# Kernel optimization log

Hardware: AMD Instinct MI355X
Metric: run time of the kernel (lower is better)

Reference implementation:

```python
import jax, jax.numpy as jnp
import numpy as np

B, T, D = 2, 2048, 1024
H, HD = 16, 64
DL, DC = 512, 256
THETA = 10000.0
LN_EPS = 1e-5


def setup_inputs() -> dict:
    key = jax.random.key(0)
    ks = jax.random.split(key, 8)
    s = 0.02
    return {
        "x": jax.random.normal(ks[0], (B, T, D), jnp.float32),
        "W_q": jax.random.normal(ks[1], (H * HD, D), jnp.float32) * s,
        "b_q": jnp.zeros((H * HD,), jnp.float32),
        "W_kvl": jax.random.normal(ks[2], (DL, D), jnp.float32) * s,
        "b_kvl": jnp.zeros((DL,), jnp.float32),
        "ts_scale": jnp.ones((DL,), jnp.float32),
        "ts_shift": jnp.zeros((DL,), jnp.float32),
        "W_comp": jax.random.normal(ks[3], (DC, DL), jnp.float32) * s,
        "W_exp": jax.random.normal(ks[4], (DL, DC), jnp.float32) * s,
        "ln_g": jnp.ones((DC,), jnp.float32),
        "ln_b": jnp.zeros((DC,), jnp.float32),
        "W_fkv": jax.random.normal(ks[5], (2 * H * HD, DL), jnp.float32) * s,
        "b_fkv": jnp.zeros((2 * H * HD,), jnp.float32),
        "W_out": jax.random.normal(ks[6], (D, H * HD), jnp.float32) * s,
        "b_out": jnp.zeros((D,), jnp.float32),
    }


def _rope_tables(t_len):
    inv_freq = 1.0 / (THETA ** (jnp.arange(0, HD, 2, dtype=jnp.float32) / HD))
    pos = jnp.arange(t_len, dtype=jnp.float32)
    freqs = pos[:, None] * inv_freq[None, :]          # [T, HD/2]
    cos = jnp.concatenate([jnp.cos(freqs)] * 2, -1)   # [T, HD]
    sin = jnp.concatenate([jnp.sin(freqs)] * 2, -1)
    return cos[None, None], sin[None, None]           # [1,1,T,HD]


def _rotate_half(z):
    return jnp.concatenate([-z[..., HD // 2:], z[..., :HD // 2]], -1)


def reference(x, W_q, b_q, W_kvl, b_kvl, ts_scale, ts_shift, W_comp, W_exp,
              ln_g, ln_b, W_fkv, b_fkv, W_out, b_out):
    # Q path: [B,T,D] -> [B,H,T,HD]
    q = (jnp.einsum('btd,ed->bte', x, W_q) + b_q).reshape(B, T, H, HD).transpose(0, 2, 1, 3)

    # KV latent + learned KVSplice bottleneck
    kvl = jnp.einsum('btd,ld->btl', x, W_kvl) + b_kvl                 # [B,T,DL]
    xt = kvl * jax.nn.softplus(ts_scale) + ts_shift
    c = jnp.einsum('btl,cl->btc', xt, W_comp)                         # [B,T,DC]
    mu = jnp.mean(c, -1, keepdims=True)
    var = jnp.mean(jnp.square(c - mu), -1, keepdims=True)
    c = (c - mu) * jax.lax.rsqrt(var + LN_EPS) * ln_g + ln_b
    dec = jnp.einsum('btc,lc->btl', c, W_exp)                         # [B,T,DL]

    # Decompress latent to K,V
    kv = jnp.einsum('btl,el->bte', dec, W_fkv) + b_fkv                # [B,T,2*H*HD]
    kv = kv.reshape(B, T, 2, H, HD).transpose(2, 0, 3, 1, 4)          # [2,B,H,T,HD]
    k, v = kv[0], kv[1]

    # RoPE
    cos, sin = _rope_tables(T)
    q = q * cos + _rotate_half(q) * sin
    k = k * cos + _rotate_half(k) * sin

    # Causal SDPA
    scale = 1.0 / np.sqrt(HD)
    scores = jnp.einsum('bhqd,bhkd->bhqk', q, k) * scale
    mask = jnp.tril(jnp.ones((T, T), bool))
    scores = jnp.where(mask, scores, jnp.float32(-1e30))
    attn = jax.nn.softmax(scores, axis=-1)
    o = jnp.einsum('bhqk,bhkd->bhqd', attn, v)
    o = o.transpose(0, 2, 1, 3).reshape(B, T, H * HD)
    return jnp.einsum('bte,de->btd', o, W_out) + b_out
```

## Files before the change

### kernel.cpp

```cpp
#include <hip/hip_runtime.h>
#include <math.h>

#define B_SZ   2
#define T_SEQ  2048
#define NH     16
#define HDIM   64
#define D_MOD  1024
#define DL     512
#define DC     256
#define MROWS  4096

typedef __attribute__((ext_vector_type(8))) short bf16x8;
typedef __attribute__((ext_vector_type(4))) float f32x4;

#define SCALE_Q 0.18033688011112042f
#define PSTR 68

static __device__ __forceinline__ unsigned short f2bf(float f) {
    union { float f; unsigned u; } v; v.f = f;
    unsigned r = v.u + 0x7fffu + ((v.u >> 16) & 1u);
    return (unsigned short)(r >> 16);
}

static __device__ __forceinline__ void gl_lds16(const unsigned short* g,
                                                unsigned short* l) {
    __builtin_amdgcn_global_load_lds(
        (const __attribute__((address_space(1))) unsigned int*)g,
        (__attribute__((address_space(3))) unsigned int*)l, 16, 0, 0);
}

__global__ __launch_bounds__(256) void cvt_bf16(
    const float* __restrict__ x,  const float* __restrict__ wq,
    const float* __restrict__ wkvl, const float* __restrict__ wcomp,
    const float* __restrict__ wexp, const float* __restrict__ wfkv,
    const float* __restrict__ wout,
    unsigned short* __restrict__ xb,  unsigned short* __restrict__ wqh,
    unsigned short* __restrict__ wkvlh, unsigned short* __restrict__ wcomph,
    unsigned short* __restrict__ wexph, unsigned short* __restrict__ wfkvh,
    unsigned short* __restrict__ wouth, float2* __restrict__ rope_tab)
{
    const int g = blockIdx.x * 256 + threadIdx.x;
    const int stride = gridDim.x * 256;
#define CVT_SEG(src, dst, n4)                                              \
    for (int i = g; i < (n4); i += stride) {                               \
        float4 v = ((const float4*)(src))[i];                              \
        unsigned short h[4] = {f2bf(v.x), f2bf(v.y), f2bf(v.z), f2bf(v.w)};\
        *(uint2*)((dst) + (size_t)i * 4) = *(uint2*)h;                     \
    }
    CVT_SEG(x, xb, 1048576)
    CVT_SEG(wq, wqh, 262144)
    CVT_SEG(wkvl, wkvlh, 131072)
    CVT_SEG(wcomp, wcomph, 32768)
    CVT_SEG(wexp, wexph, 32768)
    CVT_SEG(wfkv, wfkvh, 262144)
    CVT_SEG(wout, wouth, 262144)
#undef CVT_SEG
    for (int i = g; i < T_SEQ * 32; i += stride) {
        const int t = i >> 5, fi = i & 31;
        const float inv = __expf((float)fi * (-9.210340371976184f / 32.0f));
        float sn, cs; sincosf((float)t * inv, &sn, &cs);
        rope_tab[i] = make_float2(cs, sn);
    }
}

#define GEMM64R_PROLOG(Aptr, Wptr, Kdim)                                       \
    __shared__ unsigned short As[64 * 32];                                     \
    __shared__ unsigned short Ws[64 * 32];                                     \
    const int tid = threadIdx.x;                                               \
    const int w = tid >> 6, lane = tid & 63;                                   \
    const int l16 = lane & 15, quad = lane >> 4;                               \
    const int srow = lane >> 2, scol = (lane & 3) << 3;                        \
    const unsigned short* Ag = (Aptr) + (size_t)(m0 + w * 16 + srow) * (Kdim) + scol; \
    const unsigned short* Wg = (Wptr) + (size_t)(n0 + w * 16 + srow) * (Kdim) + scol; \
    unsigned short* Al = &As[w * 512];                                         \
    unsigned short* Wl = &Ws[w * 512];                                         \
    f32x4 acc[4];                                                              \
    _Pragma("unroll") for (int j = 0; j < 4; ++j)                              \
        acc[j] = (f32x4){0.f, 0.f, 0.f, 0.f};                                  \
    for (int k0 = 0; k0 < (Kdim); k0 += 32) {                                  \
        __syncthreads();                                                       \
        gl_lds16(Ag + k0, Al);                                                 \
        gl_lds16(Wg + k0, Wl);                                                 \
        __syncthreads();                                                       \
        const bf16x8 af = *(const bf16x8*)&As[(w * 16 + l16) * 32 + quad * 8]; \
        bf16x8 bfr[4];                                                         \
        _Pragma("unroll") for (int j = 0; j < 4; ++j)                          \
            bfr[j] = *(const bf16x8*)&Ws[(j * 16 + l16) * 32 + quad * 8];      \
        _Pragma("unroll") for (int j = 0; j < 4; ++j)                          \
            acc[j] = __builtin_amdgcn_mfma_f32_16x16x32_bf16(af, bfr[j], acc[j], 0, 0, 0); \
    }

__global__ __launch_bounds__(256) void gemm_qxt(
    const unsigned short* __restrict__ A, const unsigned short* __restrict__ Wq,
    const unsigned short* __restrict__ Wkvl,
    const float* __restrict__ b_q, const float* __restrict__ b_kvl,
    const float* __restrict__ ts_scale, const float* __restrict__ ts_shift,
    const float2* __restrict__ tab,
    unsigned short* __restrict__ qh, unsigned short* __restrict__ xt)
{
    const int m0 = blockIdx.x * 64;
    const bool is_q = (blockIdx.y < 16);
    const int n0 = is_q ? blockIdx.y * 64 : (blockIdx.y - 16) * 64;
    const unsigned short* W = is_q ? Wq : Wkvl;

    GEMM64R_PROLOG(A, W, D_MOD)

    if (is_q) {
#pragma unroll
        for (int j = 0; j < 4; ++j) {
            const int col = n0 + j * 16 + l16;
            const int h = col >> 6, hd = col & 63;
            const float bv = b_q[col];
            const float bvp = b_q[col ^ 32];
            const float sgn = (hd < 32) ? -1.f : 1.f;
#pragma unroll
            for (int reg = 0; reg < 4; ++reg) {
                const int row = m0 + w * 16 + quad * 4 + reg;
                const int b = row >> 11, t = row & (T_SEQ - 1);
                const float2 cssn = tab[t * 32 + (hd & 31)];
                const float v  = acc[j][reg] + bv;
                const float vp = acc[j ^ 2][reg] + bvp;
                const float r = (v * cssn.x + sgn * vp * cssn.y) * SCALE_Q;
                qh[(((size_t)b * NH + h) * T_SEQ + t) * HDIM + hd] = f2bf(r);
            }
        }
    } else {
#pragma unroll
        for (int j = 0; j < 4; ++j) {
            const int col = n0 + j * 16 + l16;
            const float bv = b_kvl[col];
            const float sp_s = log1pf(expf(ts_scale[col]));
            const float sp_t = ts_shift[col];
#pragma unroll
            for (int reg = 0; reg < 4; ++reg) {
                const int row = m0 + w * 16 + quad * 4 + reg;
                const float val = (acc[j][reg] + bv) * sp_s + sp_t;
                xt[(size_t)row * DL + col] = f2bf(val);
            }
        }
    }
}

__global__ __launch_bounds__(256) void gemm_kv(
    const unsigned short* __restrict__ A, const unsigned short* __restrict__ W,
    const float* __restrict__ bias, const float2* __restrict__ tab,
    unsigned short* __restrict__ kh, unsigned short* __restrict__ vth)
{
    const int m0 = blockIdx.x * 64, n0 = blockIdx.y * 64;

    GEMM64R_PROLOG(A, W, DL)

    if (n0 < 1024) {
#pragma unroll
        for (int j = 0; j < 4; ++j) {
            const int col = n0 + j * 16 + l16;
            const int h = (col >> 6) & 15, hd = col & 63;
            const float bv = bias[col];
            const float bvp = bias[col ^ 32];
            const float sgn = (hd < 32) ? -1.f : 1.f;
#pragma unroll
            for (int reg = 0; reg < 4; ++reg) {
                const int row = m0 + w * 16 + quad * 4 + reg;
                const int b = row >> 11, t = row & (T_SEQ - 1);
                const float2 cssn = tab[t * 32 + (hd & 31)];
                const float v  = acc[j][reg] + bv;
                const float vp = acc[j ^ 2][reg] + bvp;
                const float r = v * cssn.x + sgn * vp * cssn.y;
                kh[(((size_t)b * NH + h) * T_SEQ + t) * HDIM + hd] = f2bf(r);
            }
        }
    } else {
#pragma unroll
        for (int j = 0; j < 4; ++j) {
            const int col = n0 + j * 16 + l16;
            const int cv = col - 1024;
            const int h = cv >> 6, hd = cv & 63;
            const float bv = bias[col];
            unsigned short hv[4];
            const int r0 = m0 + w * 16 + quad * 4;
            const int b = r0 >> 11, t0 = r0 & (T_SEQ - 1);
#pragma unroll
            for (int reg = 0; reg < 4; ++reg)
                hv[reg] = f2bf(acc[j][reg] + bv);
            *(uint2*)&vth[(((size_t)b * NH + h) * HDIM + hd) * T_SEQ + t0] =
                *(uint2*)hv;
        }
    }
}

__global__ __launch_bounds__(256) void gemm_out(
    const unsigned short* __restrict__ A, const unsigned short* __restrict__ W,
    const float* __restrict__ bias, float* __restrict__ C)
{
    const int m0 = blockIdx.x * 64, n0 = blockIdx.y * 64;

    GEMM64R_PROLOG(A, W, D_MOD)

#pragma unroll
    for (int j = 0; j < 4; ++j) {
        const int col = n0 + j * 16 + l16;
        const float bv = bias[col];
#pragma unroll
        for (int reg = 0; reg < 4; ++reg) {
            const int row = m0 + w * 16 + quad * 4 + reg;
            C[(size_t)row * D_MOD + col] = acc[j][reg] + bv;
        }
    }
}

__global__ __launch_bounds__(256) void gemm_cb(
    const unsigned short* __restrict__ A, const unsigned short* __restrict__ Wc,
    const unsigned short* __restrict__ We,
    const float* __restrict__ g, const float* __restrict__ bta,
    unsigned short* __restrict__ dec)
{
    __shared__ unsigned short As[16 * 32];
    __shared__ unsigned short Ws[256 * 32];
    __shared__ unsigned short Cs[16 * 260];
    __shared__ float redS[4][16];
    __shared__ float redQ[4][16];

    const int tid = threadIdx.x;
    const int w = tid >> 6, lane = tid & 63;
    const int l16 = lane & 15, quad = lane >> 4;
    const int m0 = blockIdx.x * 16;

    const int srow = lane >> 2, scol = (lane & 3) << 3;
    const unsigned short* Ag = A + (size_t)(m0 + srow) * DL + scol;
    const unsigned short* Wg = Wc + (size_t)(w * 64 + srow) * DL + scol;

    f32x4 acc[4];
#pragma unroll
    for (int j = 0; j < 4; ++j) acc[j] = (f32x4){0.f, 0.f, 0.f, 0.f};

    for (int k0 = 0; k0 < DL; k0 += 32) {
        __syncthreads();
        if (w == 0) gl_lds16(Ag + k0, &As[0]);
#pragma unroll
        for (int c = 0; c < 4; ++c)
            gl_lds16(Wg + (size_t)(c * 16) * DL + k0, &Ws[(w * 64 + c * 16) * 32]);
        __syncthreads();

        const bf16x8 af = *(const bf16x8*)&As[l16 * 32 + quad * 8];
        bf16x8 bfr[4];
#pragma unroll
        for (int j = 0; j < 4; ++j)
            bfr[j] = *(const bf16x8*)&Ws[(w * 64 + j * 16 + l16) * 32 + quad * 8];
#pragma unroll
        for (int j = 0; j < 4; ++j)
            acc[j] = __builtin_amdgcn_mfma_f32_16x16x32_bf16(af, bfr[j], acc[j], 0, 0, 0);
    }

    float s[4], q2[4];
#pragma unroll
    for (int reg = 0; reg < 4; ++reg) {
        float sv = (acc[0][reg] + acc[1][reg]) + (acc[2][reg] + acc[3][reg]);
        float qv = (acc[0][reg] * acc[0][reg] + acc[1][reg] * acc[1][reg]) +
                   (acc[2][reg] * acc[2][reg] + acc[3][reg] * acc[3][reg]);
#pragma unroll
        for (int off = 1; off < 16; off <<= 1) {
            sv += __shfl_xor(sv, off);
            qv += __shfl_xor(qv, off);
        }
        s[reg] = sv; q2[reg] = qv;
    }
    if (l16 == 0) {
#pragma unroll
        for (int reg = 0; reg < 4; ++reg) {
            redS[w][quad * 4 + reg] = s[reg];
            redQ[w][quad * 4 + reg] = q2[reg];
        }
    }
    __syncthreads();

#pragma unroll
    for (int reg = 0; reg < 4; ++reg) {
        const int r = quad * 4 + reg;
        const float sum = (redS[0][r] + redS[1][r]) + (redS[2][r] + redS[3][r]);
        const float sq  = (redQ[0][r] + redQ[1][r]) + (redQ[2][r] + redQ[3][r]);
        const float mu  = sum * (1.0f / DC);
        const float var = sq * (1.0f / DC) - mu * mu;
        const float rstd = rsqrtf(var + 1e-5f);
#pragma unroll
        for (int j = 0; j < 4; ++j) {
            const int col = w * 64 + j * 16 + l16;
            const float val = (acc[j][reg] - mu) * rstd * g[col] + bta[col];
            Cs[r * 260 + col] = f2bf(val);
        }
    }
    __syncthreads();

    bf16x8 a2[8];
#pragma unroll
    for (int kk = 0; kk < 8; ++kk)
        a2[kk] = *(const bf16x8*)&Cs[l16 * 260 + kk * 32 + quad * 8];

#pragma unroll
    for (int j = 0; j < 8; ++j) {
        f32x4 acc2 = (f32x4){0.f, 0.f, 0.f, 0.f};
        const unsigned short* Bg = We + (size_t)(w * 128 + j * 16 + l16) * DC + quad * 8;
#pragma unroll
        for (int kk = 0; kk < 8; ++kk) {
            const bf16x8 b2 = *(const bf16x8*)(Bg + kk * 32);
            acc2 = __builtin_amdgcn_mfma_f32_16x16x32_bf16(a2[kk], b2, acc2, 0, 0, 0);
        }
        const int col = w * 128 + j * 16 + l16;
#pragma unroll
        for (int reg = 0; reg < 4; ++reg)
            dec[(size_t)(m0 + quad * 4 + reg) * DL + col] = f2bf(acc2[reg]);
    }
}

__global__ __launch_bounds__(256, 3) void flash_mfma(
    const unsigned short* __restrict__ q, const unsigned short* __restrict__ k,
    const unsigned short* __restrict__ vt, unsigned short* __restrict__ o)
{
    __shared__ unsigned short Ks[64 * 72];
    __shared__ unsigned short Vs[64 * 72];
    __shared__ unsigned short Ps[64 * PSTR];

    const int bh = blockIdx.x & 31;
    const int j  = 31 - (blockIdx.x >> 5);
    const int q0 = j * 64;
    const int tid = threadIdx.x;
    const int w = tid >> 6, lane = tid & 63;
    const int l16 = lane & 15, quad = lane >> 4;
    const int rbase = q0 + w * 16;

    bf16x8 qf[2];
#pragma unroll
    for (int kk = 0; kk < 2; ++kk)
        qf[kk] = *(const bf16x8*)(q + ((size_t)bh * T_SEQ + rbase + l16) * HDIM + kk * 32 + quad * 8);

    f32x4 of[4];
    float lrow[4];
#pragma unroll
    for (int dt = 0; dt < 4; ++dt) of[dt] = (f32x4){0.f, 0.f, 0.f, 0.f};
#pragma unroll
    for (int r = 0; r < 4; ++r) lrow[r] = 0.f;

    const int ldr = tid >> 2;
    const int ldc = (tid & 3) * 16;
    const unsigned short* kgb = k + ((size_t)bh * T_SEQ + ldr) * HDIM + ldc;
    const unsigned short* vgb = vt + ((size_t)bh * HDIM + ldr) * T_SEQ + ldc;

    const int kend = (j + 1) * 64;
    for (int k0 = 0; k0 < kend; k0 += 64) {
        __syncthreads();
        {
            const unsigned short* kg = kgb + (size_t)k0 * HDIM;
            *(bf16x8*)&Ks[ldr * 72 + ldc]     = *(const bf16x8*)kg;
            *(bf16x8*)&Ks[ldr * 72 + ldc + 8] = *(const bf16x8*)(kg + 8);
            const unsigned short* vg = vgb + k0;
            *(bf16x8*)&Vs[ldr * 72 + ldc]     = *(const bf16x8*)vg;
            *(bf16x8*)&Vs[ldr * 72 + ldc + 8] = *(const bf16x8*)(vg + 8);
        }
        __syncthreads();

        bf16x8 kf[4][2];
#pragma unroll
        for (int nt = 0; nt < 4; ++nt)
#pragma unroll
            for (int kk = 0; kk < 2; ++kk)
                kf[nt][kk] = *(const bf16x8*)&Ks[(nt * 16 + l16) * 72 + kk * 32 + quad * 8];

        f32x4 sf[4];
#pragma unroll
        for (int nt = 0; nt < 4; ++nt) {
            sf[nt] = (f32x4){0.f, 0.f, 0.f, 0.f};
#pragma unroll
            for (int kk = 0; kk < 2; ++kk)
                sf[nt] = __builtin_amdgcn_mfma_f32_16x16x32_bf16(qf[kk], kf[nt][kk], sf[nt], 0, 0, 0);
        }

        const bool need_mask = (k0 + 63) > rbase;
#pragma unroll
        for (int reg = 0; reg < 4; ++reg) {
            float a0 = sf[0][reg], a1 = sf[1][reg], a2 = sf[2][reg], a3 = sf[3][reg];
            if (need_mask) {
                const int tq = rbase + quad * 4 + reg;
                if (k0 +      l16 > tq) a0 = -1e30f;
                if (k0 + 16 + l16 > tq) a1 = -1e30f;
                if (k0 + 32 + l16 > tq) a2 = -1e30f;
                if (k0 + 48 + l16 > tq) a3 = -1e30f;
            }
            union { float f; unsigned u; } u0, u1, u2, u3;
            u0.f = exp2f(a0); u1.f = exp2f(a1);
            u2.f = exp2f(a2); u3.f = exp2f(a3);
            const int prow = (w * 16 + quad * 4 + reg) * PSTR + l16;
            Ps[prow]      = (unsigned short)(u0.u >> 16);
            Ps[prow + 16] = (unsigned short)(u1.u >> 16);
            Ps[prow + 32] = (unsigned short)(u2.u >> 16);
            Ps[prow + 48] = (unsigned short)(u3.u >> 16);
            u0.u &= 0xffff0000u; u1.u &= 0xffff0000u;
            u2.u &= 0xffff0000u; u3.u &= 0xffff0000u;
            lrow[reg] += (u0.f + u1.f) + (u2.f + u3.f);
        }

        bf16x8 vf[4][2];
#pragma unroll
        for (int dt = 0; dt < 4; ++dt)
#pragma unroll
            for (int kk = 0; kk < 2; ++kk)
                vf[dt][kk] = *(const bf16x8*)&Vs[(dt * 16 + l16) * 72 + kk * 32 + quad * 8];

        bf16x8 pf[2];
#pragma unroll
        for (int kk = 0; kk < 2; ++kk)
            pf[kk] = *(const bf16x8*)&Ps[(w * 16 + l16) * PSTR + kk * 32 + quad * 8];
#pragma unroll
        for (int dt = 0; dt < 4; ++dt)
#pragma unroll
            for (int kk = 0; kk < 2; ++kk)
                of[dt] = __builtin_amdgcn_mfma_f32_16x16x32_bf16(pf[kk], vf[dt][kk], of[dt], 0, 0, 0);
    }

    const int b = bh >> 4, h = bh & 15;
#pragma unroll
    for (int reg = 0; reg < 4; ++reg) {
        float l = lrow[reg];
        l += __shfl_xor(l, 1);
        l += __shfl_xor(l, 2);
        l += __shfl_xor(l, 4);
        l += __shfl_xor(l, 8);
        const float inv = 1.0f / l;
        const int t = rbase + quad * 4 + reg;
#pragma unroll
        for (int dt = 0; dt < 4; ++dt)
            o[((size_t)b * T_SEQ + t) * (NH * HDIM) + h * HDIM + dt * 16 + l16] =
                f2bf(of[dt][reg] * inv);
    }
}

extern "C" void kernel_launch(void* const* d_in, const int* in_sizes, int n_in,
                              void* d_out, int out_size, void* d_ws, size_t ws_size,
                              hipStream_t stream)
{
    (void)in_sizes; (void)n_in; (void)out_size; (void)ws_size;

    const float* x        = (const float*)d_in[0];
    const float* W_q      = (const float*)d_in[1];
    const float* b_q      = (const float*)d_in[2];
    const float* W_kvl    = (const float*)d_in[3];
    const float* b_kvl    = (const float*)d_in[4];
    const float* ts_scale = (const float*)d_in[5];
    const float* ts_shift = (const float*)d_in[6];
    const float* W_comp   = (const float*)d_in[7];
    const float* W_exp    = (const float*)d_in[8];
    const float* ln_g     = (const float*)d_in[9];
    const float* ln_b     = (const float*)d_in[10];
    const float* W_fkv    = (const float*)d_in[11];
    const float* b_fkv    = (const float*)d_in[12];
    const float* W_out    = (const float*)d_in[13];
    const float* b_out    = (const float*)d_in[14];
    float* out = (float*)d_out;

    char* p = (char*)d_ws;
    unsigned short* xb     = (unsigned short*)p;             p += 8  * 1024 * 1024;
    unsigned short* wqh    = (unsigned short*)p;             p += 2  * 1024 * 1024;
    unsigned short* wkvlh  = (unsigned short*)p;             p += 1  * 1024 * 1024;
    unsigned short* wcomph = (unsigned short*)p;             p += 256 * 1024;
    unsigned short* wexph  = (unsigned short*)p;             p += 256 * 1024;
    unsigned short* wfkvh  = (unsigned short*)p;             p += 2  * 1024 * 1024;
    unsigned short* wouth  = (unsigned short*)p;             p += 2  * 1024 * 1024;
    unsigned short* qh     = (unsigned short*)p;             p += 8  * 1024 * 1024;
    unsigned short* kh     = (unsigned short*)p;             p += 8  * 1024 * 1024;
    unsigned short* vth    = (unsigned short*)p;             p += 8  * 1024 * 1024;
    unsigned short* xt     = (unsigned short*)p;             p += 4  * 1024 * 1024;
    unsigned short* dec    = (unsigned short*)p;             p += 4  * 1024 * 1024;
    unsigned short* ob     = (unsigned short*)p;             p += 8  * 1024 * 1024;
    float2*         tab    = (float2*)p;                     p += 512 * 1024;

    const dim3 blk(256);

    cvt_bf16<<<1024, blk, 0, stream>>>(x, W_q, W_kvl, W_comp, W_exp, W_fkv, W_out,
                                       xb, wqh, wkvlh, wcomph, wexph, wfkvh, wouth,
                                       tab);

    gemm_qxt<<<dim3(64, 24), blk, 0, stream>>>(
        xb, wqh, wkvlh, b_q, b_kvl, ts_scale, ts_shift, tab, qh, xt);

    gemm_cb<<<256, blk, 0, stream>>>(
        xt, wcomph, wexph, ln_g, ln_b, dec);

    gemm_kv<<<dim3(64, 32), blk, 0, stream>>>(
        dec, wfkvh, b_fkv, tab, kh, vth);

    flash_mfma<<<1024, blk, 0, stream>>>(qh, kh, vth, ob);

    gemm_out<<<dim3(64, 16), blk, 0, stream>>>(
        ob, wouth, b_out, out);
}
```

Before: 250.0 us.

## Deepen GEMM K-tile to 64 with XOR swizzle and split compress/expand kernels

The shared 64x64 GEMM prolog now stages 64-wide K slices with an XOR-swizzled LDS layout, halving barrier pairs per K step and aiming to reduce LDS bank conflicts. The fused compress+LayerNorm+expand kernel is split in two: LN output goes to a bf16 buffer, and a separate tiled GEMM does the expansion. The old expansion read W_exp straight from global memory inside every 16-row block. The flash kernel's P buffer stride also changes from 68 to 72. The cost is an extra launch and an extra intermediate round trip through global memory.

```diff
diff --git a/kernel.cpp b/kernel.cpp
--- a/kernel.cpp
+++ b/kernel.cpp
@@ -14,7 +14,6 @@
 typedef __attribute__((ext_vector_type(4))) float f32x4;
 
 #define SCALE_Q 0.18033688011112042f
-#define PSTR 68
 
 static __device__ __forceinline__ unsigned short f2bf(float f) {
     union { float f; unsigned u; } v; v.f = f;
@@ -64,30 +63,44 @@
 }
 
 #define GEMM64R_PROLOG(Aptr, Wptr, Kdim)                                       \
-    __shared__ unsigned short As[64 * 32];                                     \
-    __shared__ unsigned short Ws[64 * 32];                                     \
+    __shared__ unsigned short As[64 * 64];                                     \
+    __shared__ unsigned short Ws[64 * 64];                                     \
     const int tid = threadIdx.x;                                               \
     const int w = tid >> 6, lane = tid & 63;                                   \
     const int l16 = lane & 15, quad = lane >> 4;                               \
-    const int srow = lane >> 2, scol = (lane & 3) << 3;                        \
-    const unsigned short* Ag = (Aptr) + (size_t)(m0 + w * 16 + srow) * (Kdim) + scol; \
-    const unsigned short* Wg = (Wptr) + (size_t)(n0 + w * 16 + srow) * (Kdim) + scol; \
-    unsigned short* Al = &As[w * 512];                                         \
-    unsigned short* Wl = &Ws[w * 512];                                         \
+    const int sw8 = ((lane & 7) ^ ((lane >> 3) & 7)) << 3;                     \
+    const int srow = lane >> 3;                                                \
+    const unsigned short* Ag0 = (Aptr) + (size_t)(m0 + w * 16 + srow) * (Kdim) + sw8;      \
+    const unsigned short* Ag1 = (Aptr) + (size_t)(m0 + w * 16 + 8 + srow) * (Kdim) + sw8;  \
+    const unsigned short* Wg0 = (Wptr) + (size_t)(n0 + w * 16 + srow) * (Kdim) + sw8;      \
+    const unsigned short* Wg1 = (Wptr) + (size_t)(n0 + w * 16 + 8 + srow) * (Kdim) + sw8;  \
+    unsigned short* Al0 = &As[(w * 16) * 64];                                  \
+    unsigned short* Al1 = &As[(w * 16 + 8) * 64];                              \
+    unsigned short* Wl0 = &Ws[(w * 16) * 64];                                  \
+    unsigned short* Wl1 = &Ws[(w * 16 + 8) * 64];                              \
+    const int xh = (l16 & 7);                                                  \
     f32x4 acc[4];                                                              \
     _Pragma("unroll") for (int j = 0; j < 4; ++j)                              \
         acc[j] = (f32x4){0.f, 0.f, 0.f, 0.f};                                  \
-    for (int k0 = 0; k0 < (Kdim); k0 += 32) {                                  \
+    for (int k0 = 0; k0 < (Kdim); k0 += 64) {                                  \
         __syncthreads();                                                       \
-        gl_lds16(Ag + k0, Al);                                                 \
-        gl_lds16(Wg + k0, Wl);                                                 \
+        gl_lds16(Ag0 + k0, Al0);                                               \
+        gl_lds16(Ag1 + k0, Al1);                                               \
+        gl_lds16(Wg0 + k0, Wl0);                                               \
+        gl_lds16(Wg1 + k0, Wl1);                                               \
         __syncthreads();                                                       \
-        const bf16x8 af = *(const bf16x8*)&As[(w * 16 + l16) * 32 + quad * 8]; \
-        bf16x8 bfr[4];                                                         \
+        bf16x8 af[2], bfr[4][2];                                               \
+        _Pragma("unroll") for (int kk = 0; kk < 2; ++kk)                       \
+            af[kk] = *(const bf16x8*)&As[(w * 16 + l16) * 64 +                 \
+                                         (((kk * 4 + quad) ^ xh) << 3)];       \
         _Pragma("unroll") for (int j = 0; j < 4; ++j)                          \
-            bfr[j] = *(const bf16x8*)&Ws[(j * 16 + l16) * 32 + quad * 8];      \
-        _Pragma("unroll") for (int j = 0; j < 4; ++j)                          \
-            acc[j] = __builtin_amdgcn_mfma_f32_16x16x32_bf16(af, bfr[j], acc[j], 0, 0, 0); \
+            _Pragma("unroll") for (int kk = 0; kk < 2; ++kk)                   \
+                bfr[j][kk] = *(const bf16x8*)&Ws[(j * 16 + l16) * 64 +         \
+                                             (((kk * 4 + quad) ^ xh) << 3)];   \
+        _Pragma("unroll") for (int kk = 0; kk < 2; ++kk)                       \
+            _Pragma("unroll") for (int j = 0; j < 4; ++j)                      \
+                acc[j] = __builtin_amdgcn_mfma_f32_16x16x32_bf16(              \
+                    af[kk], bfr[j][kk], acc[j], 0, 0, 0);                      \
     }
 
 __global__ __launch_bounds__(256) void gemm_qxt(
@@ -208,15 +221,32 @@
     }
 }
 
-__global__ __launch_bounds__(256) void gemm_cb(
-    const unsigned short* __restrict__ A, const unsigned short* __restrict__ Wc,
-    const unsigned short* __restrict__ We,
+__global__ __launch_bounds__(256) void gemm_b(
+    const unsigned short* __restrict__ A, const unsigned short* __restrict__ W,
+    unsigned short* __restrict__ dec)
+{
+    const int m0 = blockIdx.x * 64, n0 = blockIdx.y * 64;
+
+    GEMM64R_PROLOG(A, W, DC)
+
+#pragma unroll
+    for (int j = 0; j < 4; ++j) {
+        const int col = n0 + j * 16 + l16;
+#pragma unroll
+        for (int reg = 0; reg < 4; ++reg) {
+            const int row = m0 + w * 16 + quad * 4 + reg;
+            dec[(size_t)row * DL + col] = f2bf(acc[j][reg]);
+        }
+    }
+}
+
+__global__ __launch_bounds__(256) void gemm_c_ln(
+    const unsigned short* __restrict__ A, const unsigned short* __restrict__ W,
     const float* __restrict__ g, const float* __restrict__ bta,
-    unsigned short* __restrict__ dec)
+    unsigned short* __restrict__ outb)
 {
     __shared__ unsigned short As[16 * 32];
     __shared__ unsigned short Ws[256 * 32];
-    __shared__ unsigned short Cs[16 * 260];
     __shared__ float redS[4][16];
     __shared__ float redQ[4][16];
 
@@ -227,7 +257,7 @@
 
     const int srow = lane >> 2, scol = (lane & 3) << 3;
     const unsigned short* Ag = A + (size_t)(m0 + srow) * DL + scol;
-    const unsigned short* Wg = Wc + (size_t)(w * 64 + srow) * DL + scol;
+    const unsigned short* Wg = W + (size_t)(w * 64 + srow) * DL + scol;
 
     f32x4 acc[4];
 #pragma unroll
@@ -285,29 +315,8 @@
         for (int j = 0; j < 4; ++j) {
             const int col = w * 64 + j * 16 + l16;
             const float val = (acc[j][reg] - mu) * rstd * g[col] + bta[col];
-            Cs[r * 260 + col] = f2bf(val);
-        }
-    }
-    __syncthreads();
-
-    bf16x8 a2[8];
-#pragma unroll
-    for (int kk = 0; kk < 8; ++kk)
-        a2[kk] = *(const bf16x8*)&Cs[l16 * 260 + kk * 32 + quad * 8];
-
-#pragma unroll
-    for (int j = 0; j < 8; ++j) {
-        f32x4 acc2 = (f32x4){0.f, 0.f, 0.f, 0.f};
-        const unsigned short* Bg = We + (size_t)(w * 128 + j * 16 + l16) * DC + quad * 8;
-#pragma unroll
-        for (int kk = 0; kk < 8; ++kk) {
-            const bf16x8 b2 = *(const bf16x8*)(Bg + kk * 32);
-            acc2 = __builtin_amdgcn_mfma_f32_16x16x32_bf16(a2[kk], b2, acc2, 0, 0, 0);
-        }
-        const int col = w * 128 + j * 16 + l16;
-#pragma unroll
-        for (int reg = 0; reg < 4; ++reg)
-            dec[(size_t)(m0 + quad * 4 + reg) * DL + col] = f2bf(acc2[reg]);
+            outb[(size_t)(m0 + r) * DC + col] = f2bf(val);
+        }
     }
 }
 
@@ -317,7 +326,7 @@
 {
     __shared__ unsigned short Ks[64 * 72];
     __shared__ unsigned short Vs[64 * 72];
-    __shared__ unsigned short Ps[64 * PSTR];
+    __shared__ unsigned short Ps[64 * 72];
 
     const int bh = blockIdx.x & 31;
     const int j  = 31 - (blockIdx.x >> 5);
@@ -387,7 +396,7 @@
             union { float f; unsigned u; } u0, u1, u2, u3;
             u0.f = exp2f(a0); u1.f = exp2f(a1);
             u2.f = exp2f(a2); u3.f = exp2f(a3);
-            const int prow = (w * 16 + quad * 4 + reg) * PSTR + l16;
+            const int prow = (w * 16 + quad * 4 + reg) * 72 + l16;
             Ps[prow]      = (unsigned short)(u0.u >> 16);
             Ps[prow + 16] = (unsigned short)(u1.u >> 16);
             Ps[prow + 32] = (unsigned short)(u2.u >> 16);
@@ -407,7 +416,7 @@
         bf16x8 pf[2];
 #pragma unroll
         for (int kk = 0; kk < 2; ++kk)
-            pf[kk] = *(const bf16x8*)&Ps[(w * 16 + l16) * PSTR + kk * 32 + quad * 8];
+            pf[kk] = *(const bf16x8*)&Ps[(w * 16 + l16) * 72 + kk * 32 + quad * 8];
 #pragma unroll
         for (int dt = 0; dt < 4; ++dt)
 #pragma unroll
@@ -467,6 +476,7 @@
     unsigned short* kh     = (unsigned short*)p;             p += 8  * 1024 * 1024;
     unsigned short* vth    = (unsigned short*)p;             p += 8  * 1024 * 1024;
     unsigned short* xt     = (unsigned short*)p;             p += 4  * 1024 * 1024;
+    unsigned short* cbh    = (unsigned short*)p;             p += 2  * 1024 * 1024;
     unsigned short* dec    = (unsigned short*)p;             p += 4  * 1024 * 1024;
     unsigned short* ob     = (unsigned short*)p;             p += 8  * 1024 * 1024;
     float2*         tab    = (float2*)p;                     p += 512 * 1024;
@@ -480,8 +490,11 @@
     gemm_qxt<<<dim3(64, 24), blk, 0, stream>>>(
         xb, wqh, wkvlh, b_q, b_kvl, ts_scale, ts_shift, tab, qh, xt);
 
-    gemm_cb<<<256, blk, 0, stream>>>(
-        xt, wcomph, wexph, ln_g, ln_b, dec);
+    gemm_c_ln<<<256, blk, 0, stream>>>(
+        xt, wcomph, ln_g, ln_b, cbh);
+
+    gemm_b<<<dim3(64, 8), blk, 0, stream>>>(
+        cbh, wexph, dec);
 
     gemm_kv<<<dim3(64, 32), blk, 0, stream>>>(
         dec, wfkvh, b_fkv, tab, kh, vth);
```

Result: faster. 220.9 us (-11.6%).
